# Optimization experiments

Hardware: AMD Instinct MI355X
Metric: run time of the kernel (lower is better)

The kernel has to match this reference:

```python
import jax, jax.numpy as jnp
import numpy as np

B, N, D = 2048, 128, 32   # samples, features, per-feature embed dim
H = 8                     # num_head
ND = N * D                # flattened width = 4096
U = D * N // H            # per-head units = 512
DH = D // H               # per-head output feature dim = 4


def setup_inputs() -> dict:
    key = jax.random.key(0)
    k_x, k_q, k_k, k_v, k_o = jax.random.split(key, 5)
    scale_w = 0.02  # keep QK^T logits in a sane range for softmax
    x = jax.random.normal(k_x, (B, N, D), dtype=jnp.float32)
    Wq = jax.random.normal(k_q, (H, ND, U), dtype=jnp.float32) * scale_w
    Wk = jax.random.normal(k_k, (H, ND, U), dtype=jnp.float32) * scale_w
    Wv = jax.random.normal(k_v, (H, ND, U), dtype=jnp.float32) * scale_w
    Wo = jax.random.normal(k_o, (D, D), dtype=jnp.float32) * (1.0 / np.sqrt(D))
    return {"x": x, "Wq": Wq, "Wk": Wk, "Wv": Wv, "Wo": Wo}


def reference(x, Wq, Wk, Wv, Wo):
    b, n, d = x.shape
    scale = d ** (-0.5)          # note: original scales by feature dim d, not head dim
    xf = x.reshape(b, n * d)     # (b, nd); the leading 1 axis in TF is vacuous
    # Batched per-head projections (collapses the Python head loop into one GEMM each)
    q = jnp.einsum('bf,hfu->hbu', xf, Wq)   # (H, b, U)
    k = jnp.einsum('bf,hfu->hbu', xf, Wk)   # (H, b, U)
    v = jnp.einsum('bf,hfu->hbu', xf, Wv)   # (H, b, U)
    scores = jax.nn.softmax(jnp.einsum('hbu,hcu->hbc', q, k) * scale, axis=-1)  # (H, b, b)
    av = jnp.einsum('hbc,hcu->hbu', scores, v)              # (H, b, U)
    # per-head reshape (b, U) -> (b, n, d/H), then concat heads along last dim
    av = av.reshape(H, b, n, d // H)                         # (H, b, n, dh)
    concat = jnp.transpose(av, (1, 2, 0, 3)).reshape(b, n, d)  # (b, n, d)
    return concat @ Wo  # dropout rate is 0 -> identity
```

## Files before the change

kernel.cpp:

```cpp
#include <hip/hip_runtime.h>
#include <stdint.h>

typedef short    s16x8 __attribute__((ext_vector_type(8)));
typedef float    f32x4 __attribute__((ext_vector_type(4)));
typedef uint32_t u32x4 __attribute__((ext_vector_type(4)));
typedef unsigned short u16x4 __attribute__((ext_vector_type(4)));

__device__ __forceinline__ uint16_t f2bf(float f) {
  union { float f; uint32_t u; } v; v.f = f;
  uint32_t r = v.u + 0x7fffu + ((v.u >> 16) & 1u);
  return (uint16_t)(r >> 16);
}
__device__ __forceinline__ float bf2f(uint16_t h) {
  union { uint32_t u; float f; } v; v.u = ((uint32_t)h) << 16;
  return v.f;
}

__global__ __launch_bounds__(256) void cvt_x(const float* __restrict__ x,
                                             uint16_t* __restrict__ xf) {
  size_t i = ((size_t)blockIdx.x * 256 + threadIdx.x) * 4;
  f32x4 v = *(const f32x4*)(x + i);
  u16x4 o = { f2bf(v.x), f2bf(v.y), f2bf(v.z), f2bf(v.w) };
  *(u16x4*)(xf + i) = o;
}

__global__ __launch_bounds__(256) void wtrans(const float* __restrict__ W0,
                                              const float* __restrict__ W1,
                                              const float* __restrict__ W2,
                                              uint16_t* __restrict__ Wt) {
  const int z = blockIdx.z;
  const float* W = (z < 8 ? W0 : (z < 16 ? W1 : W2)) + (size_t)(z & 7) * (4096 * 512);
  const int f0 = blockIdx.x * 32, u0 = blockIdx.y * 32;
  __shared__ float t[32][33];
  const int tid = threadIdx.x;
  {
    const int fi = tid >> 3, uu = (tid & 7) * 4;
    f32x4 v = *(const f32x4*)(W + (size_t)(f0 + fi) * 512 + u0 + uu);
    t[fi][uu] = v.x; t[fi][uu + 1] = v.y; t[fi][uu + 2] = v.z; t[fi][uu + 3] = v.w;
  }
  __syncthreads();
  {
    const int ui = tid >> 3, ff = (tid & 7) * 4;
    u16x4 o = { f2bf(t[ff][ui]), f2bf(t[ff + 1][ui]),
                f2bf(t[ff + 2][ui]), f2bf(t[ff + 3][ui]) };
    *(u16x4*)&Wt[((size_t)z * 512 + u0 + ui) * 4096 + f0 + ff] = o;
  }
}

template <int MODE>
__global__ __launch_bounds__(256, 2) void gemm_bt(
    const uint16_t* __restrict__ A, size_t sAz,
    const uint16_t* __restrict__ B, size_t sBz,
    void* __restrict__ Cout, size_t sCz, int K, int ldc,
    float scale, float expC, const float* __restrict__ inv_rs) {
  const int tid = threadIdx.x;
  const int wave = tid >> 6, lane = tid & 63;
  const int quad = lane >> 4, l16 = lane & 15;
  const int wrow = (wave >> 1) * 64, wcol = (wave & 1) * 64;
  const int m0 = blockIdx.y * 128, n0 = blockIdx.x * 128;
  const int z = blockIdx.z;
  A += (size_t)z * sAz;
  B += (size_t)z * sBz;

  __shared__ uint16_t lA[128 * 40];
  __shared__ uint16_t lB[128 * 40];

  f32x4 acc[4][4];
#pragma unroll
  for (int i = 0; i < 4; i++)
#pragma unroll
    for (int j = 0; j < 4; j++) acc[i][j] = f32x4{0.f, 0.f, 0.f, 0.f};

  const int srow = tid >> 2;
  const int scol = (tid & 3) * 8;
  const uint16_t* ga = A + (size_t)(m0 + srow) * K + scol;
  const uint16_t* gb = B + (size_t)(n0 + srow) * K + scol;
  const size_t row64 = (size_t)64 * K;
  uint16_t* wA = &lA[srow * 40 + scol];
  uint16_t* wB = &lB[srow * 40 + scol];

  for (int k0 = 0; k0 < K; k0 += 32) {
    u32x4 a0 = *(const u32x4*)(ga);
    u32x4 a1 = *(const u32x4*)(ga + row64);
    u32x4 b0 = *(const u32x4*)(gb);
    u32x4 b1 = *(const u32x4*)(gb + row64);
    ga += 32; gb += 32;
    __syncthreads();
    *(u32x4*)wA = a0;
    *(u32x4*)(wA + 64 * 40) = a1;
    *(u32x4*)wB = b0;
    *(u32x4*)(wB + 64 * 40) = b1;
    __syncthreads();
    s16x8 af[4], bfr[4];
#pragma unroll
    for (int i = 0; i < 4; i++)
      af[i] = *(const s16x8*)&lA[(wrow + i * 16 + l16) * 40 + quad * 8];
#pragma unroll
    for (int j = 0; j < 4; j++)
      bfr[j] = *(const s16x8*)&lB[(wcol + j * 16 + l16) * 40 + quad * 8];
#pragma unroll
    for (int i = 0; i < 4; i++)
#pragma unroll
      for (int j = 0; j < 4; j++)
        acc[i][j] = __builtin_amdgcn_mfma_f32_16x16x32_bf16(af[i], bfr[j], acc[i][j], 0, 0, 0);
  }

  const int mb = m0 + wrow + quad * 4;
  const int nb = n0 + wcol + l16;
  if (MODE == 0) {
    uint16_t* C = (uint16_t*)Cout + (size_t)z * sCz;
#pragma unroll
    for (int i = 0; i < 4; i++)
#pragma unroll
      for (int j = 0; j < 4; j++)
#pragma unroll
        for (int r = 0; r < 4; r++)
          C[(size_t)(mb + i * 16 + r) * ldc + (nb + j * 16)] = f2bf(acc[i][j][r]);
  } else if (MODE == 1) {
    uint16_t* C = (uint16_t*)Cout + (size_t)z * sCz;
#pragma unroll
    for (int i = 0; i < 4; i++)
#pragma unroll
      for (int j = 0; j < 4; j++) {
        u16x4 o = { f2bf(acc[i][j][0]), f2bf(acc[i][j][1]),
                    f2bf(acc[i][j][2]), f2bf(acc[i][j][3]) };
        *(u16x4*)&C[(size_t)(nb + j * 16) * ldc + (mb + i * 16)] = o;
      }
  } else if (MODE == 2) {
    uint16_t* C = (uint16_t*)Cout + (size_t)z * sCz;
#pragma unroll
    for (int i = 0; i < 4; i++)
#pragma unroll
      for (int j = 0; j < 4; j++)
#pragma unroll
        for (int r = 0; r < 4; r++)
          C[(size_t)(mb + i * 16 + r) * ldc + (nb + j * 16)] =
              f2bf(__expf(fmaf(acc[i][j][r], scale, -expC)));
  } else {
    float* C = (float*)Cout + (size_t)z * sCz;
    const float* ir = inv_rs + z * 2048;
#pragma unroll
    for (int i = 0; i < 4; i++)
#pragma unroll
      for (int r = 0; r < 4; r++) {
        float w = ir[mb + i * 16 + r];
#pragma unroll
        for (int j = 0; j < 4; j++)
          C[(size_t)(mb + i * 16 + r) * ldc + (nb + j * 16)] = acc[i][j][r] * w;
      }
  }
}

__global__ __launch_bounds__(256) void rowsum(const uint16_t* __restrict__ P,
                                              float* __restrict__ inv_rs) {
  const int tid = threadIdx.x;
  const uint16_t* row = P + (size_t)blockIdx.x * 2048 + tid * 8;
  u32x4 v = *(const u32x4*)row;
  float s = 0.f;
#pragma unroll
  for (int i = 0; i < 4; i++) {
    uint32_t w = v[i];
    s += bf2f((uint16_t)(w & 0xffffu)) + bf2f((uint16_t)(w >> 16));
  }
#pragma unroll
  for (int off = 32; off > 0; off >>= 1) s += __shfl_down(s, off, 64);
  __shared__ float ps[4];
  if ((tid & 63) == 0) ps[tid >> 6] = s;
  __syncthreads();
  if (tid == 0) inv_rs[blockIdx.x] = 1.0f / (ps[0] + ps[1] + ps[2] + ps[3]);
}

__global__ __launch_bounds__(256) void out_proj(const float* __restrict__ av,
                                                const float* __restrict__ Wo,
                                                float* __restrict__ out) {
  __shared__ float lw[1024];
  const int tid = threadIdx.x;
#pragma unroll
  for (int i = 0; i < 4; i++) lw[tid + i * 256] = Wo[tid + i * 256];
  __syncthreads();
  const int p = blockIdx.x * 256 + tid;
  const int b = p >> 7, n = p & 127;
  float c[32];
#pragma unroll
  for (int h = 0; h < 8; h++) {
    f32x4 v = *(const f32x4*)(av + ((size_t)h * 2048 + b) * 512 + n * 4);
    c[h * 4] = v.x; c[h * 4 + 1] = v.y; c[h * 4 + 2] = v.z; c[h * 4 + 3] = v.w;
  }
  float o[32];
#pragma unroll
  for (int d = 0; d < 32; d++) o[d] = 0.f;
#pragma unroll
  for (int j = 0; j < 32; j++) {
    float cj = c[j];
#pragma unroll
    for (int d = 0; d < 32; d++) o[d] = fmaf(cj, lw[j * 32 + d], o[d]);
  }
  float* dst = out + (size_t)p * 32;
#pragma unroll
  for (int i = 0; i < 8; i++) {
    f32x4 v = { o[i * 4], o[i * 4 + 1], o[i * 4 + 2], o[i * 4 + 3] };
    *(f32x4*)(dst + i * 4) = v;
  }
}

extern "C" void kernel_launch(void* const* d_in, const int* in_sizes, int n_in,
                              void* d_out, int out_size, void* d_ws, size_t ws_size,
                              hipStream_t stream) {
  const float* x  = (const float*)d_in[0];
  const float* Wq = (const float*)d_in[1];
  const float* Wk = (const float*)d_in[2];
  const float* Wv = (const float*)d_in[3];
  const float* Wo = (const float*)d_in[4];
  float* out = (float*)d_out;

  uint8_t* ws = (uint8_t*)d_ws;
  uint16_t* Wt = (uint16_t*)(ws);
  uint16_t* P  = (uint16_t*)(ws);
  float*    av = (float*)(ws + 67108864);
  uint16_t* xf = (uint16_t*)(ws + 100663296);
  uint16_t* q  = (uint16_t*)(ws + 117440512);
  uint16_t* kk = (uint16_t*)(ws + 134217728);
  uint16_t* vt = (uint16_t*)(ws + 150994944);
  float*   irs = (float*)(ws + 167772160);

  const size_t WtH = (size_t)512 * 4096;
  const float scale = 0.17677669529663687f;

  cvt_x<<<8192, 256, 0, stream>>>(x, xf);
  wtrans<<<dim3(128, 16, 24), 256, 0, stream>>>(Wq, Wk, Wv, Wt);

  gemm_bt<0><<<dim3(4, 16, 8), 256, 0, stream>>>(xf, 0, Wt, WtH,
      q,  (size_t)2048 * 512, 4096, 512, 0.f, 0.f, nullptr);
  gemm_bt<0><<<dim3(4, 16, 8), 256, 0, stream>>>(xf, 0, Wt + 8 * WtH, WtH,
      kk, (size_t)2048 * 512, 4096, 512, 0.f, 0.f, nullptr);
  gemm_bt<1><<<dim3(4, 16, 8), 256, 0, stream>>>(xf, 0, Wt + 16 * WtH, WtH,
      vt, (size_t)512 * 2048, 4096, 2048, 0.f, 0.f, nullptr);

  gemm_bt<2><<<dim3(16, 16, 8), 256, 0, stream>>>(q, (size_t)2048 * 512,
      kk, (size_t)2048 * 512, P, (size_t)2048 * 2048, 512, 2048, scale, 30.0f, nullptr);

  rowsum<<<16384, 256, 0, stream>>>(P, irs);

  gemm_bt<3><<<dim3(4, 16, 8), 256, 0, stream>>>(P, (size_t)2048 * 2048,
      vt, (size_t)512 * 2048, av, (size_t)2048 * 512, 2048, 512, 0.f, 0.f, irs);

  out_proj<<<1024, 256, 0, stream>>>(av, Wo, out);
}
```

Baseline: 666.7 us.

## Fuse QKV projections, fold rowsum into score epilogue, use direct global-to-LDS loads

Merges the three Q/K/V projection GEMMs into one launch over 24 z-slices, with Q and K written contiguously and V stored transposed. The separate rowsum pass is removed: the exp-score epilogue accumulates bf16-rounded row sums through shuffles and atomicAdd into a buffer zeroed by a new small kernel. The GEMM tile loads now use global_load_lds into an XOR-swizzled, unpadded LDS layout instead of going through registers. This removes launches and one full pass over the 2048x2048 P matrix per head, but adds atomics and depends on the swizzle being correct.

```diff
diff --git a/kernel.cpp b/kernel.cpp
--- a/kernel.cpp
+++ b/kernel.cpp
@@ -14,6 +14,12 @@
 __device__ __forceinline__ float bf2f(uint16_t h) {
   union { uint32_t u; float f; } v; v.u = ((uint32_t)h) << 16;
   return v.f;
+}
+
+__device__ __forceinline__ void gld16(const void* g, void* l) {
+  __builtin_amdgcn_global_load_lds(
+      (const __attribute__((address_space(1))) void*)g,
+      (__attribute__((address_space(3))) void*)l, 16, 0, 0);
 }
 
 __global__ __launch_bounds__(256) void cvt_x(const float* __restrict__ x,
@@ -47,12 +53,16 @@
   }
 }
 
+__global__ __launch_bounds__(256) void zero_rs(float* __restrict__ rs) {
+  rs[blockIdx.x * 256 + threadIdx.x] = 0.f;
+}
+
 template <int MODE>
 __global__ __launch_bounds__(256, 2) void gemm_bt(
     const uint16_t* __restrict__ A, size_t sAz,
     const uint16_t* __restrict__ B, size_t sBz,
-    void* __restrict__ Cout, size_t sCz, int K, int ldc,
-    float scale, float expC, const float* __restrict__ inv_rs) {
+    void* __restrict__ C0, void* __restrict__ C1,
+    int K, float scale, float* __restrict__ rs) {
   const int tid = threadIdx.x;
   const int wave = tid >> 6, lane = tid & 63;
   const int quad = lane >> 4, l16 = lane & 15;
@@ -62,8 +72,8 @@
   A += (size_t)z * sAz;
   B += (size_t)z * sBz;
 
-  __shared__ uint16_t lA[128 * 40];
-  __shared__ uint16_t lB[128 * 40];
+  __shared__ __align__(16) uint16_t lA[128 * 32];
+  __shared__ __align__(16) uint16_t lB[128 * 32];
 
   f32x4 acc[4][4];
 #pragma unroll
@@ -71,33 +81,33 @@
 #pragma unroll
     for (int j = 0; j < 4; j++) acc[i][j] = f32x4{0.f, 0.f, 0.f, 0.f};
 
-  const int srow = tid >> 2;
-  const int scol = (tid & 3) * 8;
-  const uint16_t* ga = A + (size_t)(m0 + srow) * K + scol;
-  const uint16_t* gb = B + (size_t)(n0 + srow) * K + scol;
+  const int r0 = wave * 16 + (lane >> 2);
+  const int cg = ((lane & 3) ^ ((lane >> 2) & 3)) * 8;
+  const uint16_t* gA = A + (size_t)(m0 + r0) * K + cg;
+  const uint16_t* gB = B + (size_t)(n0 + r0) * K + cg;
   const size_t row64 = (size_t)64 * K;
-  uint16_t* wA = &lA[srow * 40 + scol];
-  uint16_t* wB = &lB[srow * 40 + scol];
+  uint16_t* sA0 = &lA[wave * 512];
+  uint16_t* sA1 = &lA[2048 + wave * 512];
+  uint16_t* sB0 = &lB[wave * 512];
+  uint16_t* sB1 = &lB[2048 + wave * 512];
+
+  const int fsw = (quad ^ (l16 & 3)) * 8;
 
   for (int k0 = 0; k0 < K; k0 += 32) {
-    u32x4 a0 = *(const u32x4*)(ga);
-    u32x4 a1 = *(const u32x4*)(ga + row64);
-    u32x4 b0 = *(const u32x4*)(gb);
-    u32x4 b1 = *(const u32x4*)(gb + row64);
-    ga += 32; gb += 32;
     __syncthreads();
-    *(u32x4*)wA = a0;
-    *(u32x4*)(wA + 64 * 40) = a1;
-    *(u32x4*)wB = b0;
-    *(u32x4*)(wB + 64 * 40) = b1;
+    gld16(gA, sA0);
+    gld16(gA + row64, sA1);
+    gld16(gB, sB0);
+    gld16(gB + row64, sB1);
+    gA += 32; gB += 32;
     __syncthreads();
     s16x8 af[4], bfr[4];
 #pragma unroll
     for (int i = 0; i < 4; i++)
-      af[i] = *(const s16x8*)&lA[(wrow + i * 16 + l16) * 40 + quad * 8];
+      af[i] = *(const s16x8*)&lA[(wrow + i * 16 + l16) * 32 + fsw];
 #pragma unroll
     for (int j = 0; j < 4; j++)
-      bfr[j] = *(const s16x8*)&lB[(wcol + j * 16 + l16) * 40 + quad * 8];
+      bfr[j] = *(const s16x8*)&lB[(wcol + j * 16 + l16) * 32 + fsw];
 #pragma unroll
     for (int i = 0; i < 4; i++)
 #pragma unroll
@@ -107,67 +117,77 @@
 
   const int mb = m0 + wrow + quad * 4;
   const int nb = n0 + wcol + l16;
-  if (MODE == 0) {
-    uint16_t* C = (uint16_t*)Cout + (size_t)z * sCz;
+  if (MODE == 4) {
+    if (z < 16) {
+      uint16_t* C = (uint16_t*)C0 + ((size_t)z << 20);
+#pragma unroll
+      for (int i = 0; i < 4; i++)
+#pragma unroll
+        for (int j = 0; j < 4; j++)
+#pragma unroll
+          for (int r = 0; r < 4; r++)
+            C[(size_t)(mb + i * 16 + r) * 512 + (nb + j * 16)] = f2bf(acc[i][j][r]);
+    } else {
+      uint16_t* C = (uint16_t*)C1 + ((size_t)(z - 16) << 20);
+#pragma unroll
+      for (int i = 0; i < 4; i++)
+#pragma unroll
+        for (int j = 0; j < 4; j++) {
+          u16x4 o = { f2bf(acc[i][j][0]), f2bf(acc[i][j][1]),
+                      f2bf(acc[i][j][2]), f2bf(acc[i][j][3]) };
+          *(u16x4*)&((uint16_t*)C)[(size_t)(nb + j * 16) * 2048 + (mb + i * 16)] = o;
+        }
+    }
+  } else if (MODE == 2) {
+    uint16_t* C = (uint16_t*)C0 + ((size_t)z << 22);
+    float* rz = rs + (z << 11);
+    float si[4][4];
+#pragma unroll
+    for (int i = 0; i < 4; i++)
+#pragma unroll
+      for (int r = 0; r < 4; r++) si[i][r] = 0.f;
 #pragma unroll
     for (int i = 0; i < 4; i++)
 #pragma unroll
       for (int j = 0; j < 4; j++)
 #pragma unroll
+        for (int r = 0; r < 4; r++) {
+          float e = __expf(fmaf(acc[i][j][r], scale, -30.0f));
+          uint16_t hb = f2bf(e);
+          C[(size_t)(mb + i * 16 + r) * 2048 + (nb + j * 16)] = hb;
+          si[i][r] += bf2f(hb);
+        }
+#pragma unroll
+    for (int i = 0; i < 4; i++)
+#pragma unroll
+      for (int r = 0; r < 4; r++) {
+        float s = si[i][r];
+        s += __shfl_xor(s, 1);
+        s += __shfl_xor(s, 2);
+        s += __shfl_xor(s, 4);
+        s += __shfl_xor(s, 8);
+        si[i][r] = s;
+      }
+    if (l16 == 0) {
+#pragma unroll
+      for (int i = 0; i < 4; i++)
+#pragma unroll
         for (int r = 0; r < 4; r++)
-          C[(size_t)(mb + i * 16 + r) * ldc + (nb + j * 16)] = f2bf(acc[i][j][r]);
-  } else if (MODE == 1) {
-    uint16_t* C = (uint16_t*)Cout + (size_t)z * sCz;
-#pragma unroll
-    for (int i = 0; i < 4; i++)
-#pragma unroll
-      for (int j = 0; j < 4; j++) {
-        u16x4 o = { f2bf(acc[i][j][0]), f2bf(acc[i][j][1]),
-                    f2bf(acc[i][j][2]), f2bf(acc[i][j][3]) };
-        *(u16x4*)&C[(size_t)(nb + j * 16) * ldc + (mb + i * 16)] = o;
+          atomicAdd(&rz[mb + i * 16 + r], si[i][r]);
+    }
+  } else {
+    float* C = (float*)C0 + ((size_t)z << 20);
+    const float* rz = rs + (z << 11);
+#pragma unroll
+    for (int i = 0; i < 4; i++)
+#pragma unroll
+      for (int r = 0; r < 4; r++) {
+        float w = 1.0f / rz[mb + i * 16 + r];
+#pragma unroll
+        for (int j = 0; j < 4; j++)
+          C[(size_t)(mb + i * 16 + r) * 512 + (nb + j * 16)] = acc[i][j][r] * w;
       }
-  } else if (MODE == 2) {
-    uint16_t* C = (uint16_t*)Cout + (size_t)z * sCz;
-#pragma unroll
-    for (int i = 0; i < 4; i++)
-#pragma unroll
-      for (int j = 0; j < 4; j++)
-#pragma unroll
-        for (int r = 0; r < 4; r++)
-          C[(size_t)(mb + i * 16 + r) * ldc + (nb + j * 16)] =
-              f2bf(__expf(fmaf(acc[i][j][r], scale, -expC)));
-  } else {
-    float* C = (float*)Cout + (size_t)z * sCz;
-    const float* ir = inv_rs + z * 2048;
-#pragma unroll
-    for (int i = 0; i < 4; i++)
-#pragma unroll
-      for (int r = 0; r < 4; r++) {
-        float w = ir[mb + i * 16 + r];
-#pragma unroll
-        for (int j = 0; j < 4; j++)
-          C[(size_t)(mb + i * 16 + r) * ldc + (nb + j * 16)] = acc[i][j][r] * w;
-      }
-  }
-}
-
-__global__ __launch_bounds__(256) void rowsum(const uint16_t* __restrict__ P,
-                                              float* __restrict__ inv_rs) {
-  const int tid = threadIdx.x;
-  const uint16_t* row = P + (size_t)blockIdx.x * 2048 + tid * 8;
-  u32x4 v = *(const u32x4*)row;
-  float s = 0.f;
-#pragma unroll
-  for (int i = 0; i < 4; i++) {
-    uint32_t w = v[i];
-    s += bf2f((uint16_t)(w & 0xffffu)) + bf2f((uint16_t)(w >> 16));
-  }
-#pragma unroll
-  for (int off = 32; off > 0; off >>= 1) s += __shfl_down(s, off, 64);
-  __shared__ float ps[4];
-  if ((tid & 63) == 0) ps[tid >> 6] = s;
-  __syncthreads();
-  if (tid == 0) inv_rs[blockIdx.x] = 1.0f / (ps[0] + ps[1] + ps[2] + ps[3]);
+  }
 }
 
 __global__ __launch_bounds__(256) void out_proj(const float* __restrict__ av,
@@ -219,30 +239,26 @@
   float*    av = (float*)(ws + 67108864);
   uint16_t* xf = (uint16_t*)(ws + 100663296);
   uint16_t* q  = (uint16_t*)(ws + 117440512);
-  uint16_t* kk = (uint16_t*)(ws + 134217728);
   uint16_t* vt = (uint16_t*)(ws + 150994944);
-  float*   irs = (float*)(ws + 167772160);
+  float*    rs = (float*)(ws + 167772160);
 
   const size_t WtH = (size_t)512 * 4096;
   const float scale = 0.17677669529663687f;
 
   cvt_x<<<8192, 256, 0, stream>>>(x, xf);
   wtrans<<<dim3(128, 16, 24), 256, 0, stream>>>(Wq, Wk, Wv, Wt);
-
-  gemm_bt<0><<<dim3(4, 16, 8), 256, 0, stream>>>(xf, 0, Wt, WtH,
-      q,  (size_t)2048 * 512, 4096, 512, 0.f, 0.f, nullptr);
-  gemm_bt<0><<<dim3(4, 16, 8), 256, 0, stream>>>(xf, 0, Wt + 8 * WtH, WtH,
-      kk, (size_t)2048 * 512, 4096, 512, 0.f, 0.f, nullptr);
-  gemm_bt<1><<<dim3(4, 16, 8), 256, 0, stream>>>(xf, 0, Wt + 16 * WtH, WtH,
-      vt, (size_t)512 * 2048, 4096, 2048, 0.f, 0.f, nullptr);
-
-  gemm_bt<2><<<dim3(16, 16, 8), 256, 0, stream>>>(q, (size_t)2048 * 512,
-      kk, (size_t)2048 * 512, P, (size_t)2048 * 2048, 512, 2048, scale, 30.0f, nullptr);
-
-  rowsum<<<16384, 256, 0, stream>>>(P, irs);
-
-  gemm_bt<3><<<dim3(4, 16, 8), 256, 0, stream>>>(P, (size_t)2048 * 2048,
-      vt, (size_t)512 * 2048, av, (size_t)2048 * 512, 2048, 512, 0.f, 0.f, irs);
+  zero_rs<<<64, 256, 0, stream>>>(rs);
+
+  gemm_bt<4><<<dim3(4, 16, 24), 256, 0, stream>>>(
+      xf, 0, Wt, WtH, q, vt, 4096, 0.f, nullptr);
+
+  gemm_bt<2><<<dim3(16, 16, 8), 256, 0, stream>>>(
+      q, (size_t)2048 * 512, q + (size_t)8 * 2048 * 512, (size_t)2048 * 512,
+      P, nullptr, 512, scale, rs);
+
+  gemm_bt<3><<<dim3(4, 16, 8), 256, 0, stream>>>(
+      P, (size_t)2048 * 2048, vt, (size_t)512 * 2048,
+      av, nullptr, 2048, 0.f, rs);
 
   out_proj<<<1024, 256, 0, stream>>>(av, Wo, out);
 }
```

Result: faster. 635.3 us (-4.7%).
